# Kernel tuning notes

Hardware: AMD Instinct MI355X
Metric: run time of the kernel (lower is better)

The kernel has to match this reference:

```python
import jax, jax.numpy as jnp
import numpy as np

B, S, H = 512, 200, 256

def setup_inputs() -> dict:
    key = jax.random.key(0)
    ks = jax.random.split(key, 7)
    scale = 1.0 / np.sqrt(H)
    return {
        "all_memory": jax.random.normal(ks[0], (B, S, H), dtype=jnp.float32),
        "last_memory": jax.random.normal(ks[1], (B, H), dtype=jnp.float32),
        "U": jax.random.normal(ks[2], (H, H), dtype=jnp.float32) * scale,   # U_meta weight
        "W": jax.random.normal(ks[3], (H, H), dtype=jnp.float32) * scale,   # W_meta weight
        "V": jax.random.normal(ks[4], (H, 1), dtype=jnp.float32) * scale,   # V_meta weight (stored as [H,1])
        "MetaW": jax.random.normal(ks[5], (4, H), dtype=jnp.float32) * scale,  # Meta weight
        "Metab": jax.random.normal(ks[6], (4,), dtype=jnp.float32) * scale,    # Meta bias ('multiple' mode)
    }

def reference(all_memory, last_memory, U, W, V, MetaW, Metab):
    # U_meta(all_memory): [B,S,H]; W_meta(last_memory): [B,H] broadcast over S
    a = jnp.einsum('bsh,kh->bsk', all_memory, U)
    l = jnp.einsum('bh,kh->bk', last_memory, W)
    # additive attention score: V_meta(tanh(a + l)) -> [B,S]
    scores = jnp.einsum('bsh,h->bs', jnp.tanh(a + l[:, None, :]), V[:, 0])
    alpha = jax.nn.softmax(scores, axis=1)  # softmax over seq dim
    pooled = jnp.einsum('bs,bsh->bh', alpha, all_memory)  # weighted sum of values
    return pooled @ MetaW.T + Metab  # [B, 4]
```

## Files before the change

kernel.cpp:

```cpp
#include <hip/hip_runtime.h>
#include <hip/hip_bf16.h>
#include <math.h>

#define NB 512
#define NS 200
#define NH 256
#define TILE_S 32
#define NTILE 7
#define NCHUNK 4
#define LDSPAD 8
#define LDW (NH + LDSPAD)

#define OFF_SC 0
#define OFF_L  (NB * NS)
#define OFF_UB (OFF_L + NB * NH)
#define WS_FLOATS_PRE (OFF_UB + (NH * NH) / 2)

typedef __bf16 bf16x8 __attribute__((ext_vector_type(8)));
typedef float  f32x4  __attribute__((ext_vector_type(4)));

__device__ __forceinline__ float tanh_fast(float x) {
  float xc = fminf(fmaxf(x, -10.f), 10.f);
  float e  = __expf(2.f * xc);
  return (e - 1.f) / (e + 1.f);
}

__global__ __launch_bounds__(256)
void precompute(const float* __restrict__ lastm, const float* __restrict__ W,
                const float* __restrict__ U,
                float* __restrict__ l_ws, __bf16* __restrict__ Uswz)
{
  const int t = threadIdx.x;
  if (blockIdx.x < NB) {
    const int b = blockIdx.x;
    __shared__ float lm_sm[NH];
    lm_sm[t] = lastm[(size_t)b * NH + t];
    __syncthreads();
    const float4* wrow = (const float4*)(W + (size_t)t * NH);
    const float4* lrow = (const float4*)lm_sm;
    float a0 = 0.f, a1 = 0.f, a2 = 0.f, a3 = 0.f;
#pragma unroll 8
    for (int i = 0; i < NH / 4; ++i) {
      float4 w4 = wrow[i];
      float4 m4 = lrow[i];
      a0 = fmaf(w4.x, m4.x, a0);
      a1 = fmaf(w4.y, m4.y, a1);
      a2 = fmaf(w4.z, m4.z, a2);
      a3 = fmaf(w4.w, m4.w, a3);
    }
    l_ws[(size_t)b * NH + t] = (a0 + a1) + (a2 + a3);
  } else {
    const int id    = (blockIdx.x - NB) * 256 + t;
    const int n_blk = id >> 9;
    const int kk    = (id >> 6) & 7;
    const int lane  = id & 63;
    const int row   = n_blk * 16 + (lane & 15);
    const int col   = kk * 32 + (lane >> 4) * 8;
    const float4* s = (const float4*)(U + (size_t)row * NH + col);
    const float4 a = s[0], c = s[1];
    bf16x8 pk;
    pk[0] = (__bf16)a.x; pk[1] = (__bf16)a.y;
    pk[2] = (__bf16)a.z; pk[3] = (__bf16)a.w;
    pk[4] = (__bf16)c.x; pk[5] = (__bf16)c.y;
    pk[6] = (__bf16)c.z; pk[7] = (__bf16)c.w;
    *(bf16x8*)(Uswz + (size_t)id * 8) = pk;
  }
}

template<bool PRE>
__global__ __launch_bounds__(256, 2)
void scores_kernel(const float* __restrict__ mem,
                   const float* __restrict__ lastm,
                   const float* __restrict__ U,
                   const float* __restrict__ W,
                   const float* __restrict__ V,
                   const float* __restrict__ l_ws,
                   const __bf16* __restrict__ Uswz,
                   float* __restrict__ scores)
{
  const int blk  = blockIdx.x;
  const int b    = blk / NTILE;
  const int tile = blk - b * NTILE;
  const int s0   = tile * TILE_S;
  const int rows = min(TILE_S, NS - s0);

  const int t    = threadIdx.x;
  const int wave = t >> 6;
  const int lane = t & 63;
  const int m16  = lane & 15;
  const int quad = lane >> 4;

  __shared__ __align__(16) __bf16 mem_sm[TILE_S][LDW];
  __shared__ float swave_sm[4][TILE_S];
  __shared__ float l_sm[NH];

  if (!PRE) {
    const float4* wrow = (const float4*)(W + (size_t)t * NH);
    const float4* lrow = (const float4*)(lastm + (size_t)b * NH);
    float a0 = 0.f, a1 = 0.f, a2 = 0.f, a3 = 0.f;
#pragma unroll 8
    for (int i = 0; i < NH / 4; ++i) {
      float4 w4 = wrow[i];
      float4 m4 = lrow[i];
      a0 = fmaf(w4.x, m4.x, a0);
      a1 = fmaf(w4.y, m4.y, a1);
      a2 = fmaf(w4.z, m4.z, a2);
      a3 = fmaf(w4.w, m4.w, a3);
    }
    l_sm[t] = (a0 + a1) + (a2 + a3);
    __syncthreads();
  }

  const float4* src4 = (const float4*)(mem + ((size_t)b * NS + s0) * NH);
#pragma unroll
  for (int i = 0; i < 4; ++i) {
    const int f2  = i * 256 + t;
    const int row = f2 >> 5;
    const int c8  = (f2 & 31) * 8;
    bf16x8 pk;
    if (row < rows) {
      const float4 a = src4[f2 * 2];
      const float4 c = src4[f2 * 2 + 1];
      pk[0] = (__bf16)a.x; pk[1] = (__bf16)a.y;
      pk[2] = (__bf16)a.z; pk[3] = (__bf16)a.w;
      pk[4] = (__bf16)c.x; pk[5] = (__bf16)c.y;
      pk[6] = (__bf16)c.z; pk[7] = (__bf16)c.w;
    } else {
      pk = (bf16x8)(__bf16)0.f;
    }
    *(bf16x8*)&mem_sm[row][c8] = pk;
  }
  __syncthreads();

  float p[2][4];
#pragma unroll
  for (int mt = 0; mt < 2; ++mt)
#pragma unroll
    for (int reg = 0; reg < 4; ++reg)
      p[mt][reg] = 0.f;

  for (int chunk = 0; chunk < NCHUNK; ++chunk) {
    const int n_blk = chunk * 4 + wave;
    const int n     = n_blk * 16 + m16;

    bf16x8 u_frag[8];
    if (PRE) {
      const __bf16* uw = Uswz + ((size_t)(n_blk * 8 * 64) + lane) * 8;
#pragma unroll
      for (int kk = 0; kk < 8; ++kk)
        u_frag[kk] = *(const bf16x8*)(uw + (size_t)(kk << 9));
    } else {
      const float* urow = U + (size_t)n * NH;
#pragma unroll
      for (int kk = 0; kk < 8; ++kk) {
        const float4 lo = *(const float4*)(urow + kk * 32 + quad * 8);
        const float4 hi = *(const float4*)(urow + kk * 32 + quad * 8 + 4);
        bf16x8 f;
        f[0] = (__bf16)lo.x; f[1] = (__bf16)lo.y;
        f[2] = (__bf16)lo.z; f[3] = (__bf16)lo.w;
        f[4] = (__bf16)hi.x; f[5] = (__bf16)hi.y;
        f[6] = (__bf16)hi.z; f[7] = (__bf16)hi.w;
        u_frag[kk] = f;
      }
    }

    const float l_reg = PRE ? l_ws[(size_t)b * NH + n] : l_sm[n];
    const float v_reg = V[n];

    f32x4 acc[2];
    const f32x4 fzero = {0.f, 0.f, 0.f, 0.f};
    acc[0] = fzero; acc[1] = fzero;
#pragma unroll
    for (int kk = 0; kk < 8; ++kk) {
      const int c = kk * 32 + quad * 8;
      bf16x8 a0 = *(const bf16x8*)&mem_sm[m16][c];
      bf16x8 a1 = *(const bf16x8*)&mem_sm[16 + m16][c];
      acc[0] = __builtin_amdgcn_mfma_f32_16x16x32_bf16(a0, u_frag[kk], acc[0], 0, 0, 0);
      acc[1] = __builtin_amdgcn_mfma_f32_16x16x32_bf16(a1, u_frag[kk], acc[1], 0, 0, 0);
    }

#pragma unroll
    for (int mt = 0; mt < 2; ++mt)
#pragma unroll
      for (int reg = 0; reg < 4; ++reg)
        p[mt][reg] = fmaf(tanh_fast(acc[mt][reg] + l_reg), v_reg, p[mt][reg]);
  }

#pragma unroll
  for (int off = 1; off < 16; off <<= 1) {
#pragma unroll
    for (int mt = 0; mt < 2; ++mt)
#pragma unroll
      for (int reg = 0; reg < 4; ++reg)
        p[mt][reg] += __shfl_xor(p[mt][reg], off);
  }
  if (m16 == 0) {
#pragma unroll
    for (int mt = 0; mt < 2; ++mt)
#pragma unroll
      for (int reg = 0; reg < 4; ++reg)
        swave_sm[wave][mt * 16 + quad * 4 + reg] = p[mt][reg];
  }
  __syncthreads();

  if (t < rows)
    scores[(size_t)b * NS + s0 + t] =
        swave_sm[0][t] + swave_sm[1][t] + swave_sm[2][t] + swave_sm[3][t];
}

__global__ __launch_bounds__(512)
void softmax_pool(const float* __restrict__ scores,
                  const float* __restrict__ mem,
                  const float* __restrict__ MetaW,
                  const float* __restrict__ Metab,
                  float* __restrict__ out)
{
  const int b    = blockIdx.x;
  const int t    = threadIdx.x;
  const int wave = t >> 6;
  const int lane = t & 63;

  __shared__ float alpha_sm[NS];
  __shared__ float red_sm[8];
  __shared__ __align__(16) float part_sm[8][NH];
  __shared__ float pooled_sm[NH];

  float sv = (t < NS) ? scores[(size_t)b * NS + t] : -INFINITY;

  float wm = sv;
#pragma unroll
  for (int off = 32; off > 0; off >>= 1)
    wm = fmaxf(wm, __shfl_xor(wm, off));
  if (lane == 0) red_sm[wave] = wm;
  __syncthreads();
  float m = red_sm[0];
#pragma unroll
  for (int w = 1; w < 8; ++w) m = fmaxf(m, red_sm[w]);

  float e = (t < NS) ? __expf(sv - m) : 0.f;
  float wsum = e;
#pragma unroll
  for (int off = 32; off > 0; off >>= 1)
    wsum += __shfl_xor(wsum, off);
  __syncthreads();
  if (lane == 0) red_sm[wave] = wsum;
  __syncthreads();
  float Z = 0.f;
#pragma unroll
  for (int w = 0; w < 8; ++w) Z += red_sm[w];
  const float Zi = 1.f / Z;

  if (t < NS) alpha_sm[t] = e * Zi;
  __syncthreads();

  f32x4 acc4 = {0.f, 0.f, 0.f, 0.f};
  const f32x4* memb = (const f32x4*)(mem + (size_t)b * NS * NH);
  for (int r = wave; r < NS; r += 8) {
    const float a = alpha_sm[r];
    const f32x4 v4 = memb[(size_t)r * (NH / 4) + lane];
    acc4[0] = fmaf(a, v4[0], acc4[0]);
    acc4[1] = fmaf(a, v4[1], acc4[1]);
    acc4[2] = fmaf(a, v4[2], acc4[2]);
    acc4[3] = fmaf(a, v4[3], acc4[3]);
  }
  *(f32x4*)&part_sm[wave][lane * 4] = acc4;
  __syncthreads();

  if (t < NH) {
    float s = 0.f;
#pragma unroll
    for (int w = 0; w < 8; ++w) s += part_sm[w][t];
    pooled_sm[t] = s;
  }
  __syncthreads();

  if (wave < 4) {
    float s = 0.f;
#pragma unroll
    for (int i = 0; i < 4; ++i) {
      const int h = i * 64 + lane;
      s = fmaf(pooled_sm[h], MetaW[(size_t)wave * NH + h], s);
    }
#pragma unroll
    for (int off = 32; off > 0; off >>= 1)
      s += __shfl_down(s, off);
    if (lane == 0)
      out[b * 4 + wave] = s + Metab[wave];
  }
}

extern "C" void kernel_launch(void* const* d_in, const int* in_sizes, int n_in,
                              void* d_out, int out_size, void* d_ws, size_t ws_size,
                              hipStream_t stream) {
  const float* mem   = (const float*)d_in[0];
  const float* lastm = (const float*)d_in[1];
  const float* U     = (const float*)d_in[2];
  const float* W     = (const float*)d_in[3];
  const float* V     = (const float*)d_in[4];
  const float* MetaW = (const float*)d_in[5];
  const float* Metab = (const float*)d_in[6];
  float* out = (float*)d_out;
  float* ws  = (float*)d_ws;

  float* scores = ws + OFF_SC;

  if (ws_size >= (size_t)WS_FLOATS_PRE * sizeof(float)) {
    float*  l_ws = ws + OFF_L;
    __bf16* Uswz = (__bf16*)(ws + OFF_UB);
    hipLaunchKernelGGL(precompute, dim3(NB + 32), dim3(256), 0, stream,
                       lastm, W, U, l_ws, Uswz);
    hipLaunchKernelGGL(scores_kernel<true>, dim3(NB * NTILE), dim3(256), 0, stream,
                       mem, lastm, U, W, V, l_ws, Uswz, scores);
  } else {
    hipLaunchKernelGGL(scores_kernel<false>, dim3(NB * NTILE), dim3(256), 0, stream,
                       mem, lastm, U, W, V, (const float*)nullptr, (const __bf16*)nullptr, scores);
  }
  hipLaunchKernelGGL(softmax_pool, dim3(NB), dim3(512), 0, stream,
                     scores, mem, MetaW, Metab, out);
}
```

Baseline: 215.6 us.

## Give each wave its own sequence tile with register-resident A fragments

Restructures the scores kernel so each wave owns a full 32-row sequence tile and loops over all 16 output column blocks, loading the memory rows straight from global into bf16 register fragments. This removes the LDS staging, the block barriers and the cross-wave shared-memory reduction, and cuts the grid to a quarter of the blocks. Each wave now reads all of U per tile, which raises traffic through L2 for U, and register pressure goes up. The tanh is also changed to an exp plus hardware reciprocal form without clamping.

```diff
diff --git a/kernel.cpp b/kernel.cpp
--- a/kernel.cpp
+++ b/kernel.cpp
@@ -7,9 +7,7 @@
 #define NH 256
 #define TILE_S 32
 #define NTILE 7
-#define NCHUNK 4
-#define LDSPAD 8
-#define LDW (NH + LDSPAD)
+#define NTASK (NB * NTILE)
 
 #define OFF_SC 0
 #define OFF_L  (NB * NS)
@@ -20,9 +18,8 @@
 typedef float  f32x4  __attribute__((ext_vector_type(4)));
 
 __device__ __forceinline__ float tanh_fast(float x) {
-  float xc = fminf(fmaxf(x, -10.f), 10.f);
-  float e  = __expf(2.f * xc);
-  return (e - 1.f) / (e + 1.f);
+  float e = __expf(x + x);
+  return fmaf(-2.f, __builtin_amdgcn_rcpf(e + 1.f), 1.f);
 }
 
 __global__ __launch_bounds__(256)
@@ -78,59 +75,35 @@
                    const __bf16* __restrict__ Uswz,
                    float* __restrict__ scores)
 {
-  const int blk  = blockIdx.x;
-  const int b    = blk / NTILE;
-  const int tile = blk - b * NTILE;
+  const int wave = threadIdx.x >> 6;
+  const int lane = threadIdx.x & 63;
+  const int task = blockIdx.x * 4 + wave;
+  const int b    = task / NTILE;
+  const int tile = task - b * NTILE;
   const int s0   = tile * TILE_S;
-  const int rows = min(TILE_S, NS - s0);
-
-  const int t    = threadIdx.x;
-  const int wave = t >> 6;
-  const int lane = t & 63;
   const int m16  = lane & 15;
   const int quad = lane >> 4;
 
-  __shared__ __align__(16) __bf16 mem_sm[TILE_S][LDW];
-  __shared__ float swave_sm[4][TILE_S];
-  __shared__ float l_sm[NH];
-
-  if (!PRE) {
-    const float4* wrow = (const float4*)(W + (size_t)t * NH);
-    const float4* lrow = (const float4*)(lastm + (size_t)b * NH);
-    float a0 = 0.f, a1 = 0.f, a2 = 0.f, a3 = 0.f;
-#pragma unroll 8
-    for (int i = 0; i < NH / 4; ++i) {
-      float4 w4 = wrow[i];
-      float4 m4 = lrow[i];
-      a0 = fmaf(w4.x, m4.x, a0);
-      a1 = fmaf(w4.y, m4.y, a1);
-      a2 = fmaf(w4.z, m4.z, a2);
-      a3 = fmaf(w4.w, m4.w, a3);
-    }
-    l_sm[t] = (a0 + a1) + (a2 + a3);
-    __syncthreads();
-  }
-
-  const float4* src4 = (const float4*)(mem + ((size_t)b * NS + s0) * NH);
-#pragma unroll
-  for (int i = 0; i < 4; ++i) {
-    const int f2  = i * 256 + t;
-    const int row = f2 >> 5;
-    const int c8  = (f2 & 31) * 8;
-    bf16x8 pk;
-    if (row < rows) {
-      const float4 a = src4[f2 * 2];
-      const float4 c = src4[f2 * 2 + 1];
-      pk[0] = (__bf16)a.x; pk[1] = (__bf16)a.y;
-      pk[2] = (__bf16)a.z; pk[3] = (__bf16)a.w;
-      pk[4] = (__bf16)c.x; pk[5] = (__bf16)c.y;
-      pk[6] = (__bf16)c.z; pk[7] = (__bf16)c.w;
-    } else {
-      pk = (bf16x8)(__bf16)0.f;
-    }
-    *(bf16x8*)&mem_sm[row][c8] = pk;
-  }
-  __syncthreads();
+  const int r0 = min(s0 + m16, NS - 1);
+  const int r1 = min(s0 + 16 + m16, NS - 1);
+  const float* rp0 = mem + ((size_t)b * NS + r0) * NH + quad * 8;
+  const float* rp1 = mem + ((size_t)b * NS + r1) * NH + quad * 8;
+
+  bf16x8 a_frag[2][8];
+#pragma unroll
+  for (int kk = 0; kk < 8; ++kk) {
+    const float4 lo0 = *(const float4*)(rp0 + kk * 32);
+    const float4 hi0 = *(const float4*)(rp0 + kk * 32 + 4);
+    const float4 lo1 = *(const float4*)(rp1 + kk * 32);
+    const float4 hi1 = *(const float4*)(rp1 + kk * 32 + 4);
+    bf16x8 f0, f1;
+    f0[0] = (__bf16)lo0.x; f0[1] = (__bf16)lo0.y; f0[2] = (__bf16)lo0.z; f0[3] = (__bf16)lo0.w;
+    f0[4] = (__bf16)hi0.x; f0[5] = (__bf16)hi0.y; f0[6] = (__bf16)hi0.z; f0[7] = (__bf16)hi0.w;
+    f1[0] = (__bf16)lo1.x; f1[1] = (__bf16)lo1.y; f1[2] = (__bf16)lo1.z; f1[3] = (__bf16)lo1.w;
+    f1[4] = (__bf16)hi1.x; f1[5] = (__bf16)hi1.y; f1[6] = (__bf16)hi1.z; f1[7] = (__bf16)hi1.w;
+    a_frag[0][kk] = f0;
+    a_frag[1][kk] = f1;
+  }
 
   float p[2][4];
 #pragma unroll
@@ -139,16 +112,16 @@
     for (int reg = 0; reg < 4; ++reg)
       p[mt][reg] = 0.f;
 
-  for (int chunk = 0; chunk < NCHUNK; ++chunk) {
-    const int n_blk = chunk * 4 + wave;
-    const int n     = n_blk * 16 + m16;
+#pragma unroll 1
+  for (int n_blk = 0; n_blk < 16; ++n_blk) {
+    const int n = n_blk * 16 + m16;
 
     bf16x8 u_frag[8];
     if (PRE) {
-      const __bf16* uw = Uswz + ((size_t)(n_blk * 8 * 64) + lane) * 8;
+      const __bf16* uw = Uswz + (size_t)n_blk * 4096 + (size_t)lane * 8;
 #pragma unroll
       for (int kk = 0; kk < 8; ++kk)
-        u_frag[kk] = *(const bf16x8*)(uw + (size_t)(kk << 9));
+        u_frag[kk] = *(const bf16x8*)(uw + (kk << 9));
     } else {
       const float* urow = U + (size_t)n * NH;
 #pragma unroll
@@ -164,26 +137,31 @@
       }
     }
 
-    const float l_reg = PRE ? l_ws[(size_t)b * NH + n] : l_sm[n];
-    const float v_reg = V[n];
-
-    f32x4 acc[2];
-    const f32x4 fzero = {0.f, 0.f, 0.f, 0.f};
-    acc[0] = fzero; acc[1] = fzero;
+    float l_reg, v_reg;
+    if (PRE) {
+      l_reg = l_ws[(size_t)b * NH + n];
+    } else {
+      const float* lm = lastm + (size_t)b * NH;
+      const float* wr = W + (size_t)n * NH;
+      float a0 = 0.f;
+      for (int i = 0; i < NH; ++i) a0 = fmaf(lm[i], wr[i], a0);
+      l_reg = a0;
+    }
+    v_reg = V[n];
+
+    f32x4 acc0 = {0.f, 0.f, 0.f, 0.f};
+    f32x4 acc1 = {0.f, 0.f, 0.f, 0.f};
 #pragma unroll
     for (int kk = 0; kk < 8; ++kk) {
-      const int c = kk * 32 + quad * 8;
-      bf16x8 a0 = *(const bf16x8*)&mem_sm[m16][c];
-      bf16x8 a1 = *(const bf16x8*)&mem_sm[16 + m16][c];
-      acc[0] = __builtin_amdgcn_mfma_f32_16x16x32_bf16(a0, u_frag[kk], acc[0], 0, 0, 0);
-      acc[1] = __builtin_amdgcn_mfma_f32_16x16x32_bf16(a1, u_frag[kk], acc[1], 0, 0, 0);
-    }
-
-#pragma unroll
-    for (int mt = 0; mt < 2; ++mt)
-#pragma unroll
-      for (int reg = 0; reg < 4; ++reg)
-        p[mt][reg] = fmaf(tanh_fast(acc[mt][reg] + l_reg), v_reg, p[mt][reg]);
+      acc0 = __builtin_amdgcn_mfma_f32_16x16x32_bf16(a_frag[0][kk], u_frag[kk], acc0, 0, 0, 0);
+      acc1 = __builtin_amdgcn_mfma_f32_16x16x32_bf16(a_frag[1][kk], u_frag[kk], acc1, 0, 0, 0);
+    }
+
+#pragma unroll
+    for (int reg = 0; reg < 4; ++reg) {
+      p[0][reg] = fmaf(tanh_fast(acc0[reg] + l_reg), v_reg, p[0][reg]);
+      p[1][reg] = fmaf(tanh_fast(acc1[reg] + l_reg), v_reg, p[1][reg]);
+    }
   }
 
 #pragma unroll
@@ -194,18 +172,17 @@
       for (int reg = 0; reg < 4; ++reg)
         p[mt][reg] += __shfl_xor(p[mt][reg], off);
   }
+
   if (m16 == 0) {
 #pragma unroll
     for (int mt = 0; mt < 2; ++mt)
 #pragma unroll
-      for (int reg = 0; reg < 4; ++reg)
-        swave_sm[wave][mt * 16 + quad * 4 + reg] = p[mt][reg];
-  }
-  __syncthreads();
-
-  if (t < rows)
-    scores[(size_t)b * NS + s0 + t] =
-        swave_sm[0][t] + swave_sm[1][t] + swave_sm[2][t] + swave_sm[3][t];
+      for (int reg = 0; reg < 4; ++reg) {
+        const int r = s0 + mt * 16 + quad * 4 + reg;
+        if (r < NS)
+          scores[(size_t)b * NS + r] = p[mt][reg];
+      }
+  }
 }
 
 __global__ __launch_bounds__(512)
@@ -309,10 +286,10 @@
     __bf16* Uswz = (__bf16*)(ws + OFF_UB);
     hipLaunchKernelGGL(precompute, dim3(NB + 32), dim3(256), 0, stream,
                        lastm, W, U, l_ws, Uswz);
-    hipLaunchKernelGGL(scores_kernel<true>, dim3(NB * NTILE), dim3(256), 0, stream,
+    hipLaunchKernelGGL(scores_kernel<true>, dim3(NTASK / 4), dim3(256), 0, stream,
                        mem, lastm, U, W, V, l_ws, Uswz, scores);
   } else {
-    hipLaunchKernelGGL(scores_kernel<false>, dim3(NB * NTILE), dim3(256), 0, stream,
+    hipLaunchKernelGGL(scores_kernel<false>, dim3(NTASK / 4), dim3(256), 0, stream,
                        mem, lastm, U, W, V, (const float*)nullptr, (const __bf16*)nullptr, scores);
   }
   hipLaunchKernelGGL(softmax_pool, dim3(NB), dim3(512), 0, stream,
```

Result: slower. 222.1 us (+3.0%).
